# Kernel optimization log

Hardware: AMD Instinct MI355X
Metric: run time of the kernel (lower is better)

Reference implementation:

```python
import jax, jax.numpy as jnp
import numpy as np

B, S, D, H = 4, 2048, 1024, 16
DK = D // H
SCALE = 1.0 / np.float32(np.sqrt(DK))


def setup_inputs() -> dict:
    key = jax.random.key(0)
    ks = jax.random.split(key, 11)
    w = lambda k: (jax.random.normal(k, (D, D), jnp.float32) * 0.02)
    b = lambda k: (jax.random.normal(k, (D,), jnp.float32) * 0.02)
    return {
        "Q": jax.random.normal(ks[0], (B, S, D), jnp.float32),
        "K": jax.random.normal(ks[1], (B, S, D), jnp.float32),
        "V": jax.random.normal(ks[2], (B, S, D), jnp.float32),
        "Wq": w(ks[3]), "bq": b(ks[4]),
        "Wk": w(ks[5]), "bk": b(ks[6]),
        "Wv": w(ks[7]), "bv": b(ks[8]),
        "Wo": w(ks[9]), "bo": b(ks[10]),
        # causal mask, broadcast over batch and heads: [1,1,S,S]
        "mask": jnp.tril(jnp.ones((1, 1, S, S), dtype=bool)),
    }


def reference(Q, K, V, Wq, bq, Wk, bk, Wv, bv, Wo, bo, mask):
    def proj(x, W, bias):
        # [B,S,D] -> [B,H,S,DK]
        return (x @ W + bias).reshape(B, S, H, DK).transpose(0, 2, 1, 3)

    q = proj(Q, Wq, bq)
    k = proj(K, Wk, bk)
    v = proj(V, Wv, bv)
    scores = jnp.einsum("bhqd,bhkd->bhqk", q, k) * SCALE  # [B,H,S,S]
    scores = jnp.where(mask, scores, jnp.float32(-1e9))
    attn = jax.nn.softmax(scores, axis=-1)
    out = jnp.einsum("bhqk,bhkd->bhqd", attn, v)  # [B,H,S,DK]
    out = out.transpose(0, 2, 1, 3).reshape(B, S, D)
    return out @ Wo + bo
```

## Files before the change

kernel.cpp:

```cpp
#include <hip/hip_runtime.h>
#include <hip/hip_bf16.h>
#include <stdint.h>

#define BB 4
#define SS 2048
#define DD 1024
#define HH 16
#define DKK 64
#define MM (BB * SS)

typedef __hip_bfloat16 bf16;
typedef __attribute__((ext_vector_type(8))) short frag8;
typedef __attribute__((ext_vector_type(4))) float f32x4;

#define GLDS16(g, l)                                                        \
  __builtin_amdgcn_global_load_lds(                                         \
      (const __attribute__((address_space(1))) void*)(g),                   \
      (__attribute__((address_space(3))) void*)(l), 16, 0, 0)

#define MFMA __builtin_amdgcn_mfma_f32_16x16x32_bf16

__device__ __forceinline__ unsigned short f2bu(float f) {
  __hip_bfloat16 h = __float2bfloat16(f);
  return *reinterpret_cast<unsigned short*>(&h);
}

struct WtArgs {
  const float* s[3];
  unsigned short* d[3];
};
__global__ __launch_bounds__(256) void wtrans_kernel(WtArgs a) {
  const float* __restrict__ W = a.s[blockIdx.z];
  unsigned short* __restrict__ Wt = a.d[blockIdx.z];
  __shared__ float t[64][68];
  const int n0 = blockIdx.x * 64, k0 = blockIdx.y * 64;
  const int tid = threadIdx.x;
#pragma unroll
  for (int it = 0; it < 4; ++it) {
    const int kk = it * 16 + (tid >> 4);
    const int nn = (tid & 15) * 4;
    const float4 v = *(const float4*)&W[(size_t)(k0 + kk) * DD + n0 + nn];
    *(float4*)&t[kk][nn] = v;
  }
  __syncthreads();
#pragma unroll
  for (int it = 0; it < 2; ++it) {
    const int n = it * 32 + (tid >> 3);
    const int c = tid & 7;
    frag8 pk;
#pragma unroll
    for (int j = 0; j < 8; ++j) pk[j] = (short)f2bu(t[c * 8 + j][n]);
    *(frag8*)&Wt[(size_t)(n0 + n) * DD + k0 + c * 8] = pk;
  }
}

struct CvtArgs {
  const float* s[3];
  unsigned short* d[3];
};
__global__ __launch_bounds__(256) void cvt_kernel(CvtArgs a) {
  const float* __restrict__ src = a.s[blockIdx.y];
  unsigned short* __restrict__ dst = a.d[blockIdx.y];
  const size_t i = ((size_t)blockIdx.x * 256 + threadIdx.x) * 8;
  const float4 v0 = *(const float4*)&src[i];
  const float4 v1 = *(const float4*)&src[i + 4];
  frag8 pk;
  pk[0] = (short)f2bu(v0.x); pk[1] = (short)f2bu(v0.y);
  pk[2] = (short)f2bu(v0.z); pk[3] = (short)f2bu(v0.w);
  pk[4] = (short)f2bu(v1.x); pk[5] = (short)f2bu(v1.y);
  pk[6] = (short)f2bu(v1.z); pk[7] = (short)f2bu(v1.w);
  *(frag8*)&dst[i] = pk;
}

struct GArgs {
  const void* A[3];
  const unsigned short* W[3];
  const float* bias[3];
  void* out[3];
  float oscale[3];
  int abf16[3];
  int omode[3];
};
__global__ __launch_bounds__(256) void gemm_kernel(GArgs ga) {
  constexpr int K = DD;
  const int z = blockIdx.z;
  const void* __restrict__ Av = ga.A[z];
  const unsigned short* __restrict__ Wt = ga.W[z];
  const float* __restrict__ bias = ga.bias[z];
  void* __restrict__ outv = ga.out[z];
  const float oscale = ga.oscale[z];
  const int abf = ga.abf16[z];
  const int omode = ga.omode[z];

  __shared__ unsigned short Bs[2][128 * 64];
  __shared__ unsigned short As[2][128 * 64];
  const int tid = threadIdx.x;
  const int wave = tid >> 6, lane = tid & 63, quad = lane >> 4, l15 = lane & 15;
  const int wr = wave >> 1, wc = wave & 1;
  const int mt = blockIdx.x * 8 + (blockIdx.y >> 3);
  const int nt = blockIdx.y & 7;
  const int m0 = mt * 128, n0 = nt * 128;

  f32x4 acc[4][4] = {};
  float4 r0[4], r1[4];

  auto stageB = [&](int buf, int k0) {
#pragma unroll
    for (int c = 0; c < 4; ++c) {
      const int row = c * 32 + wave * 8 + (lane >> 3);
      const int gc = ((lane & 7) ^ (row & 7)) * 8;
      const unsigned short* g = &Wt[(size_t)(n0 + row) * K + k0 + gc];
      unsigned off = __builtin_amdgcn_readfirstlane(
          (unsigned)(buf * 16384 + (c * 32 + wave * 8) * 128));
      GLDS16(g, (char*)&Bs[0][0] + off);
    }
  };
  auto stageA16 = [&](int buf, int k0) {
    const unsigned short* A = (const unsigned short*)Av;
#pragma unroll
    for (int c = 0; c < 4; ++c) {
      const int row = c * 32 + wave * 8 + (lane >> 3);
      const int gc = ((lane & 7) ^ (row & 7)) * 8;
      const unsigned short* g = &A[(size_t)(m0 + row) * K + k0 + gc];
      unsigned off = __builtin_amdgcn_readfirstlane(
          (unsigned)(buf * 16384 + (c * 32 + wave * 8) * 128));
      GLDS16(g, (char*)&As[0][0] + off);
    }
  };
  auto loadA32 = [&](int k0) {
    const float* A = (const float*)Av;
#pragma unroll
    for (int it = 0; it < 4; ++it) {
      const int row = it * 32 + (tid >> 3);
      const int c = tid & 7;
      r0[it] = *(const float4*)&A[(size_t)(m0 + row) * K + k0 + c * 8];
      r1[it] = *(const float4*)&A[(size_t)(m0 + row) * K + k0 + c * 8 + 4];
    }
  };
  auto writeA32 = [&](int buf) {
#pragma unroll
    for (int it = 0; it < 4; ++it) {
      const int row = it * 32 + (tid >> 3);
      const int c = tid & 7;
      frag8 pk;
      pk[0] = (short)f2bu(r0[it].x); pk[1] = (short)f2bu(r0[it].y);
      pk[2] = (short)f2bu(r0[it].z); pk[3] = (short)f2bu(r0[it].w);
      pk[4] = (short)f2bu(r1[it].x); pk[5] = (short)f2bu(r1[it].y);
      pk[6] = (short)f2bu(r1[it].z); pk[7] = (short)f2bu(r1[it].w);
      *(frag8*)&As[buf][row * 64 + ((c ^ (row & 7)) * 8)] = pk;
    }
  };
  auto compute = [&](int buf) {
#pragma unroll
    for (int s = 0; s < 2; ++s) {
      frag8 af[4], bfr[4];
#pragma unroll
      for (int mi = 0; mi < 4; ++mi)
        af[mi] = *(const frag8*)&As[buf][(wr * 64 + mi * 16 + l15) * 64 +
                                         (((s * 4 + quad) ^ (l15 & 7)) * 8)];
#pragma unroll
      for (int ni = 0; ni < 4; ++ni)
        bfr[ni] = *(const frag8*)&Bs[buf][(wc * 64 + ni * 16 + l15) * 64 +
                                          (((s * 4 + quad) ^ (l15 & 7)) * 8)];
#pragma unroll
      for (int mi = 0; mi < 4; ++mi)
#pragma unroll
        for (int ni = 0; ni < 4; ++ni)
          acc[mi][ni] = MFMA(af[mi], bfr[ni], acc[mi][ni], 0, 0, 0);
    }
  };

  if (abf) {
    stageB(0, 0);
    stageA16(0, 0);
  } else {
    loadA32(0);
    stageB(0, 0);
    writeA32(0);
  }
  __syncthreads();

#pragma unroll 1
  for (int t = 0; t < 16; t += 2) {
    if (t + 1 < 16) {
      if (abf) {
        stageB(1, (t + 1) * 64);
        stageA16(1, (t + 1) * 64);
      } else {
        loadA32((t + 1) * 64);
        stageB(1, (t + 1) * 64);
      }
    }
    compute(0);
    if (!abf && t + 1 < 16) writeA32(1);
    __syncthreads();
    if (t + 2 < 16) {
      if (abf) {
        stageB(0, (t + 2) * 64);
        stageA16(0, (t + 2) * 64);
      } else {
        loadA32((t + 2) * 64);
        stageB(0, (t + 2) * 64);
      }
    }
    compute(1);
    if (!abf && t + 2 < 16) writeA32(0);
    __syncthreads();
  }

#pragma unroll
  for (int mi = 0; mi < 4; ++mi) {
#pragma unroll
    for (int ni = 0; ni < 4; ++ni) {
#pragma unroll
      for (int r = 0; r < 4; ++r) {
        const int grow = m0 + wr * 64 + mi * 16 + quad * 4 + r;
        const int gcol = n0 + wc * 64 + ni * 16 + l15;
        const float val = (acc[mi][ni][r] + bias[gcol]) * oscale;
        if (omode == 2) {
          ((float*)outv)[(size_t)grow * DD + gcol] = val;
        } else {
          const int b = grow / SS, s = grow % SS;
          const int h = gcol / DKK, dk = gcol % DKK;
          unsigned short* o = (unsigned short*)outv;
          if (omode == 0)
            o[(((size_t)(b * HH + h)) * SS + s) * DKK + dk] = f2bu(val);
          else
            o[(((size_t)(b * HH + h)) * DKK + dk) * SS + s] = f2bu(val);
        }
      }
    }
  }
}

__global__ __launch_bounds__(256) void fattn_kernel(
    const unsigned short* __restrict__ q, const unsigned short* __restrict__ k,
    const unsigned short* __restrict__ vt, unsigned short* __restrict__ ctx) {
  __shared__ unsigned short Ks[2][64 * 64];
  __shared__ unsigned short Vs[2][64 * 64];
  __shared__ unsigned short P_lds[4][16][36];
  const int tid = threadIdx.x;
  const int wave = tid >> 6, lane = tid & 63, quad = lane >> 4, l15 = lane & 15;
  const int bh = blockIdx.x & 63;
  const int tp = blockIdx.x >> 6;
  const size_t qkb = (size_t)bh * SS * DKK;
  const size_t vtb = (size_t)bh * DKK * SS;
  const int b = bh / HH, h = bh % HH;

  frag8 ones;
#pragma unroll
  for (int s = 0; s < 8; ++s) ones[s] = (short)0x3F80;

  auto stage = [&](int buf, int jt) {
#pragma unroll
    for (int c = 0; c < 2; ++c) {
      const int row = wave * 16 + c * 8 + (lane >> 3);
      const int gc = ((lane & 7) ^ (row & 7)) * 8;
      const unsigned short* g = &k[qkb + (size_t)(jt * 64 + row) * DKK + gc];
      unsigned off = __builtin_amdgcn_readfirstlane(
          (unsigned)(buf * 8192 + (wave * 16 + c * 8) * 128));
      GLDS16(g, (char*)&Ks[0][0] + off);
    }
#pragma unroll
    for (int c = 0; c < 2; ++c) {
      const int row = wave * 16 + c * 8 + (lane >> 3);
      const int gc = ((lane & 7) ^ (row & 7)) * 8;
      const unsigned short* g = &vt[vtb + (size_t)row * SS + jt * 64 + gc];
      unsigned off = __builtin_amdgcn_readfirstlane(
          (unsigned)(buf * 8192 + (wave * 16 + c * 8) * 128));
      GLDS16(g, (char*)&Vs[0][0] + off);
    }
  };

  for (int half = 0; half < 2; ++half) {
    const int t = half ? (31 - tp) : tp;
    const int q0 = t * 64 + wave * 16;

    const frag8 aq0 =
        *(const frag8*)&q[qkb + (size_t)(q0 + l15) * DKK + quad * 8];
    const frag8 aq1 =
        *(const frag8*)&q[qkb + (size_t)(q0 + l15) * DKK + 32 + quad * 8];

    f32x4 oacc[4] = {};
    f32x4 lacc = {};

    const int nT = t + 1;
    stage(0, 0);
    __syncthreads();

    for (int jt = 0; jt < nT; ++jt) {
      const int p = jt & 1;
      if (jt + 1 < nT) stage(1 - p, jt + 1);
      const bool diag = (jt == t);

#pragma unroll
      for (int jsub = 0; jsub < 2; ++jsub) {
        f32x4 sc[2];
#pragma unroll
        for (int g = 0; g < 2; ++g) {
          const int row = jsub * 32 + g * 16 + l15;
          const frag8 kf0 =
              *(const frag8*)&Ks[p][row * 64 + ((quad ^ (l15 & 7)) * 8)];
          const frag8 kf1 =
              *(const frag8*)&Ks[p][row * 64 + (((4 + quad) ^ (l15 & 7)) * 8)];
          f32x4 z = {};
          z = MFMA(aq0, kf0, z, 0, 0, 0);
          sc[g] = MFMA(aq1, kf1, z, 0, 0, 0);
        }
        float p0[4], p1[4];
        if (diag) {
          const int jg = jt * 64 + jsub * 32;
#pragma unroll
          for (int r = 0; r < 4; ++r) {
            const int ig = q0 + quad * 4 + r;
            p0[r] = (jg + l15 <= ig) ? __expf(sc[0][r]) : 0.f;
            p1[r] = (jg + 16 + l15 <= ig) ? __expf(sc[1][r]) : 0.f;
          }
        } else {
#pragma unroll
          for (int r = 0; r < 4; ++r) {
            p0[r] = __expf(sc[0][r]);
            p1[r] = __expf(sc[1][r]);
          }
        }
#pragma unroll
        for (int r = 0; r < 4; ++r) {
          P_lds[wave][quad * 4 + r][l15] = f2bu(p0[r]);
          P_lds[wave][quad * 4 + r][16 + l15] = f2bu(p1[r]);
        }
        const frag8 pa = *(const frag8*)&P_lds[wave][l15][quad * 8];
#pragma unroll
        for (int c = 0; c < 4; ++c) {
          const int vrow = c * 16 + l15;
          const int chunk = ((jsub * 4 + quad) ^ (l15 & 7));
          const frag8 vf = *(const frag8*)&Vs[p][vrow * 64 + chunk * 8];
          oacc[c] = MFMA(pa, vf, oacc[c], 0, 0, 0);
        }
        lacc = MFMA(pa, ones, lacc, 0, 0, 0);
      }
      __syncthreads();
    }

#pragma unroll
    for (int r = 0; r < 4; ++r) {
      const float inv = 1.f / lacc[r];
      const int ig = q0 + quad * 4 + r;
#pragma unroll
      for (int c = 0; c < 4; ++c)
        ctx[((size_t)(b * SS + ig)) * DD + h * DKK + c * 16 + l15] =
            f2bu(oacc[c][r] * inv);
    }
  }
}

extern "C" void kernel_launch(void* const* d_in, const int* in_sizes, int n_in,
                              void* d_out, int out_size, void* d_ws,
                              size_t ws_size, hipStream_t stream) {
  const float* Q = (const float*)d_in[0];
  const float* K = (const float*)d_in[1];
  const float* V = (const float*)d_in[2];
  const float* Wq = (const float*)d_in[3];
  const float* bq = (const float*)d_in[4];
  const float* Wk = (const float*)d_in[5];
  const float* bk = (const float*)d_in[6];
  const float* Wv = (const float*)d_in[7];
  const float* bv = (const float*)d_in[8];
  const float* Wo = (const float*)d_in[9];
  const float* bo = (const float*)d_in[10];

  const size_t NE = (size_t)MM * DD;
  unsigned short* ctx = (unsigned short*)d_ws;
  unsigned short* qp = ctx + NE;
  unsigned short* kp = qp + NE;
  unsigned short* vtp = kp + NE;
  unsigned short* Qb = vtp + NE;
  unsigned short* Kb = Qb + NE;
  unsigned short* Vb = Kb + NE;
  unsigned short* Wqt = ctx;
  unsigned short* Wkt = ctx + 1048576;
  unsigned short* Wvt = ctx + 2097152;
  unsigned short* Wot = qp;

  const bool fastQK = ws_size >= (size_t)6 * NE * sizeof(unsigned short);
  const bool fastV = ws_size >= (size_t)7 * NE * sizeof(unsigned short);

  const dim3 gg(8, 64, 3);

  WtArgs wa1;
  wa1.s[0] = Wq; wa1.s[1] = Wk; wa1.s[2] = Wv;
  wa1.d[0] = Wqt; wa1.d[1] = Wkt; wa1.d[2] = Wvt;
  wtrans_kernel<<<dim3(16, 16, 3), 256, 0, stream>>>(wa1);

  int ncvt = 0;
  CvtArgs ca;
  if (fastQK) {
    ca.s[0] = Q; ca.d[0] = Qb;
    ca.s[1] = K; ca.d[1] = Kb;
    ncvt = 2;
    if (fastV) { ca.s[2] = V; ca.d[2] = Vb; ncvt = 3; }
    cvt_kernel<<<dim3(NE / 2048, ncvt), 256, 0, stream>>>(ca);
  }

  GArgs g3;
  g3.A[0] = fastQK ? (const void*)Qb : (const void*)Q;
  g3.A[1] = fastQK ? (const void*)Kb : (const void*)K;
  g3.A[2] = fastV ? (const void*)Vb : (const void*)V;
  g3.W[0] = Wqt; g3.W[1] = Wkt; g3.W[2] = Wvt;
  g3.bias[0] = bq; g3.bias[1] = bk; g3.bias[2] = bv;
  g3.out[0] = qp; g3.out[1] = kp; g3.out[2] = vtp;
  g3.oscale[0] = 0.125f; g3.oscale[1] = 1.f; g3.oscale[2] = 1.f;
  g3.abf16[0] = fastQK ? 1 : 0; g3.abf16[1] = fastQK ? 1 : 0;
  g3.abf16[2] = fastV ? 1 : 0;
  g3.omode[0] = 0; g3.omode[1] = 0; g3.omode[2] = 1;
  gemm_kernel<<<gg, 256, 0, stream>>>(g3);

  fattn_kernel<<<dim3(BB * HH * 16), 256, 0, stream>>>(qp, kp, vtp, ctx);

  WtArgs wa2;
  wa2.s[0] = Wo; wa2.d[0] = Wot;
  wa2.s[1] = Wo; wa2.d[1] = Wot;
  wa2.s[2] = Wo; wa2.d[2] = Wot;
  wtrans_kernel<<<dim3(16, 16, 1), 256, 0, stream>>>(wa2);

  GArgs go;
  go.A[0] = (const void*)ctx; go.W[0] = Wot; go.bias[0] = bo;
  go.out[0] = (void*)d_out; go.oscale[0] = 1.f;
  go.abf16[0] = 1; go.omode[0] = 2;
  go.A[1] = go.A[0]; go.W[1] = go.W[0]; go.bias[1] = go.bias[0];
  go.out[1] = go.out[0]; go.oscale[1] = 1.f; go.abf16[1] = 1; go.omode[1] = 2;
  go.A[2] = go.A[0]; go.W[2] = go.W[0]; go.bias[2] = go.bias[0];
  go.out[2] = go.out[0]; go.oscale[2] = 1.f; go.abf16[2] = 1; go.omode[2] = 2;
  gemm_kernel<<<dim3(8, 64, 1), 256, 0, stream>>>(go);
}
```

Measured before the change: 361.9 us.

## Add BK=32 GEMM variant and widen attention blocks to 128 query rows

Adds a new bf16 GEMM kernel with K-tile of 32, a single-sync-per-step double buffer and a paired-row swizzled LDS layout, used for both projection and output GEMMs when the workspace is large enough. The attention kernel is changed to 512 threads (8 waves) covering 128 query rows per block, so each staged K/V tile is shared by twice as many waves. It also skips fully masked sub-tiles per wave and masks partially. Costs: more barriers in the GEMM and extra idle waves on diagonal tiles in attention.

```diff
diff --git a/kernel.cpp b/kernel.cpp
--- a/kernel.cpp
+++ b/kernel.cpp
@@ -81,6 +81,100 @@
   int abf16[3];
   int omode[3];
 };
+
+__global__ __launch_bounds__(256) void gemm32_kernel(GArgs ga) {
+  constexpr int K = DD;
+  const int z = blockIdx.z;
+  const unsigned short* __restrict__ A = (const unsigned short*)ga.A[z];
+  const unsigned short* __restrict__ Wt = ga.W[z];
+  const float* __restrict__ bias = ga.bias[z];
+  void* __restrict__ outv = ga.out[z];
+  const float oscale = ga.oscale[z];
+  const int omode = ga.omode[z];
+
+  __shared__ unsigned short As[2][128 * 32];
+  __shared__ unsigned short Bs[2][128 * 32];
+  const int tid = threadIdx.x;
+  const int wave = tid >> 6, lane = tid & 63, quad = lane >> 4, l15 = lane & 15;
+  const int wr = wave >> 1, wc = wave & 1;
+  const int mt = blockIdx.x * 8 + (blockIdx.y >> 3);
+  const int nt = blockIdx.y & 7;
+  const int m0 = mt * 128, n0 = nt * 128;
+
+  f32x4 acc[4][4] = {};
+
+  auto stage = [&](int buf, int k0) {
+#pragma unroll
+    for (int j = 0; j < 2; ++j) {
+      const int win = wave * 2 + j;
+      const int srl = lane >> 3;
+      const int pp = lane & 7;
+      const int p = pp ^ srl;
+      const int row = (win * 8 + srl) * 2 + (p >> 2);
+      const int c = p & 3;
+      const unsigned off = __builtin_amdgcn_readfirstlane(
+          (unsigned)(buf * 8192 + win * 1024));
+      GLDS16(&A[(size_t)(m0 + row) * K + k0 + c * 8], (char*)&As[0][0] + off);
+      GLDS16(&Wt[(size_t)(n0 + row) * K + k0 + c * 8], (char*)&Bs[0][0] + off);
+    }
+  };
+  auto compute = [&](int buf) {
+    frag8 af[4], bfr[4];
+#pragma unroll
+    for (int mi = 0; mi < 4; ++mi) {
+      const int R = wr * 64 + mi * 16 + l15;
+      const int sr = R >> 1;
+      const int pp = (((R & 1) << 2) | quad) ^ (sr & 7);
+      af[mi] = *(const frag8*)&As[buf][sr * 64 + pp * 8];
+    }
+#pragma unroll
+    for (int ni = 0; ni < 4; ++ni) {
+      const int R = wc * 64 + ni * 16 + l15;
+      const int sr = R >> 1;
+      const int pp = (((R & 1) << 2) | quad) ^ (sr & 7);
+      bfr[ni] = *(const frag8*)&Bs[buf][sr * 64 + pp * 8];
+    }
+#pragma unroll
+    for (int mi = 0; mi < 4; ++mi)
+#pragma unroll
+      for (int ni = 0; ni < 4; ++ni)
+        acc[mi][ni] = MFMA(af[mi], bfr[ni], acc[mi][ni], 0, 0, 0);
+  };
+
+  stage(0, 0);
+  __syncthreads();
+#pragma unroll 1
+  for (int t = 0; t < 32; ++t) {
+    if (t + 1 < 32) stage((t & 1) ^ 1, (t + 1) * 32);
+    compute(t & 1);
+    __syncthreads();
+  }
+
+#pragma unroll
+  for (int mi = 0; mi < 4; ++mi) {
+#pragma unroll
+    for (int ni = 0; ni < 4; ++ni) {
+#pragma unroll
+      for (int r = 0; r < 4; ++r) {
+        const int grow = m0 + wr * 64 + mi * 16 + quad * 4 + r;
+        const int gcol = n0 + wc * 64 + ni * 16 + l15;
+        const float val = (acc[mi][ni][r] + bias[gcol]) * oscale;
+        if (omode == 2) {
+          ((float*)outv)[(size_t)grow * DD + gcol] = val;
+        } else {
+          const int b = grow / SS, s = grow % SS;
+          const int h = gcol / DKK, dk = gcol % DKK;
+          unsigned short* outp = (unsigned short*)outv;
+          if (omode == 0)
+            outp[(((size_t)(b * HH + h)) * SS + s) * DKK + dk] = f2bu(val);
+          else
+            outp[(((size_t)(b * HH + h)) * DKK + dk) * SS + s] = f2bu(val);
+        }
+      }
+    }
+  }
+}
+
 __global__ __launch_bounds__(256) void gemm_kernel(GArgs ga) {
   constexpr int K = DD;
   const int z = blockIdx.z;
@@ -116,25 +210,25 @@
     }
   };
   auto stageA16 = [&](int buf, int k0) {
-    const unsigned short* A = (const unsigned short*)Av;
+    const unsigned short* Ap = (const unsigned short*)Av;
 #pragma unroll
     for (int c = 0; c < 4; ++c) {
       const int row = c * 32 + wave * 8 + (lane >> 3);
       const int gc = ((lane & 7) ^ (row & 7)) * 8;
-      const unsigned short* g = &A[(size_t)(m0 + row) * K + k0 + gc];
+      const unsigned short* g = &Ap[(size_t)(m0 + row) * K + k0 + gc];
       unsigned off = __builtin_amdgcn_readfirstlane(
           (unsigned)(buf * 16384 + (c * 32 + wave * 8) * 128));
       GLDS16(g, (char*)&As[0][0] + off);
     }
   };
   auto loadA32 = [&](int k0) {
-    const float* A = (const float*)Av;
+    const float* Ap = (const float*)Av;
 #pragma unroll
     for (int it = 0; it < 4; ++it) {
       const int row = it * 32 + (tid >> 3);
       const int c = tid & 7;
-      r0[it] = *(const float4*)&A[(size_t)(m0 + row) * K + k0 + c * 8];
-      r1[it] = *(const float4*)&A[(size_t)(m0 + row) * K + k0 + c * 8 + 4];
+      r0[it] = *(const float4*)&Ap[(size_t)(m0 + row) * K + k0 + c * 8];
+      r1[it] = *(const float4*)&Ap[(size_t)(m0 + row) * K + k0 + c * 8 + 4];
     }
   };
   auto writeA32 = [&](int buf) {
@@ -153,20 +247,20 @@
   auto compute = [&](int buf) {
 #pragma unroll
     for (int s = 0; s < 2; ++s) {
-      frag8 af[4], bfr[4];
+      frag8 a2[4], b2[4];
 #pragma unroll
       for (int mi = 0; mi < 4; ++mi)
-        af[mi] = *(const frag8*)&As[buf][(wr * 64 + mi * 16 + l15) * 64 +
+        a2[mi] = *(const frag8*)&As[buf][(wr * 64 + mi * 16 + l15) * 64 +
                                          (((s * 4 + quad) ^ (l15 & 7)) * 8)];
 #pragma unroll
       for (int ni = 0; ni < 4; ++ni)
-        bfr[ni] = *(const frag8*)&Bs[buf][(wc * 64 + ni * 16 + l15) * 64 +
-                                          (((s * 4 + quad) ^ (l15 & 7)) * 8)];
+        b2[ni] = *(const frag8*)&Bs[buf][(wc * 64 + ni * 16 + l15) * 64 +
+                                         (((s * 4 + quad) ^ (l15 & 7)) * 8)];
 #pragma unroll
       for (int mi = 0; mi < 4; ++mi)
 #pragma unroll
         for (int ni = 0; ni < 4; ++ni)
-          acc[mi][ni] = MFMA(af[mi], bfr[ni], acc[mi][ni], 0, 0, 0);
+          acc[mi][ni] = MFMA(a2[mi], b2[ni], acc[mi][ni], 0, 0, 0);
     }
   };
 
@@ -222,23 +316,23 @@
         } else {
           const int b = grow / SS, s = grow % SS;
           const int h = gcol / DKK, dk = gcol % DKK;
-          unsigned short* o = (unsigned short*)outv;
+          unsigned short* outp = (unsigned short*)outv;
           if (omode == 0)
-            o[(((size_t)(b * HH + h)) * SS + s) * DKK + dk] = f2bu(val);
+            outp[(((size_t)(b * HH + h)) * SS + s) * DKK + dk] = f2bu(val);
           else
-            o[(((size_t)(b * HH + h)) * DKK + dk) * SS + s] = f2bu(val);
+            outp[(((size_t)(b * HH + h)) * DKK + dk) * SS + s] = f2bu(val);
         }
       }
     }
   }
 }
 
-__global__ __launch_bounds__(256) void fattn_kernel(
+__global__ __launch_bounds__(512) void fattn_kernel(
     const unsigned short* __restrict__ q, const unsigned short* __restrict__ k,
     const unsigned short* __restrict__ vt, unsigned short* __restrict__ ctx) {
   __shared__ unsigned short Ks[2][64 * 64];
   __shared__ unsigned short Vs[2][64 * 64];
-  __shared__ unsigned short P_lds[4][16][36];
+  __shared__ unsigned short P_lds[8][16][36];
   const int tid = threadIdx.x;
   const int wave = tid >> 6, lane = tid & 63, quad = lane >> 4, l15 = lane & 15;
   const int bh = blockIdx.x & 63;
@@ -252,29 +346,18 @@
   for (int s = 0; s < 8; ++s) ones[s] = (short)0x3F80;
 
   auto stage = [&](int buf, int jt) {
-#pragma unroll
-    for (int c = 0; c < 2; ++c) {
-      const int row = wave * 16 + c * 8 + (lane >> 3);
-      const int gc = ((lane & 7) ^ (row & 7)) * 8;
-      const unsigned short* g = &k[qkb + (size_t)(jt * 64 + row) * DKK + gc];
-      unsigned off = __builtin_amdgcn_readfirstlane(
-          (unsigned)(buf * 8192 + (wave * 16 + c * 8) * 128));
-      GLDS16(g, (char*)&Ks[0][0] + off);
-    }
-#pragma unroll
-    for (int c = 0; c < 2; ++c) {
-      const int row = wave * 16 + c * 8 + (lane >> 3);
-      const int gc = ((lane & 7) ^ (row & 7)) * 8;
-      const unsigned short* g = &vt[vtb + (size_t)row * SS + jt * 64 + gc];
-      unsigned off = __builtin_amdgcn_readfirstlane(
-          (unsigned)(buf * 8192 + (wave * 16 + c * 8) * 128));
-      GLDS16(g, (char*)&Vs[0][0] + off);
-    }
+    const int row = wave * 8 + (lane >> 3);
+    const int gc = ((lane & 7) ^ (lane >> 3)) * 8;
+    const unsigned off =
+        __builtin_amdgcn_readfirstlane((unsigned)(buf * 8192 + wave * 1024));
+    GLDS16(&k[qkb + (size_t)(jt * 64 + row) * DKK + gc],
+           (char*)&Ks[0][0] + off);
+    GLDS16(&vt[vtb + (size_t)row * SS + jt * 64 + gc], (char*)&Vs[0][0] + off);
   };
 
   for (int half = 0; half < 2; ++half) {
-    const int t = half ? (31 - tp) : tp;
-    const int q0 = t * 64 + wave * 16;
+    const int t = half ? (15 - tp) : tp;
+    const int q0 = t * 128 + wave * 16;
 
     const frag8 aq0 =
         *(const frag8*)&q[qkb + (size_t)(q0 + l15) * DKK + quad * 8];
@@ -284,59 +367,62 @@
     f32x4 oacc[4] = {};
     f32x4 lacc = {};
 
-    const int nT = t + 1;
+    const int nT = 2 * t + 2;
     stage(0, 0);
     __syncthreads();
 
     for (int jt = 0; jt < nT; ++jt) {
       const int p = jt & 1;
       if (jt + 1 < nT) stage(1 - p, jt + 1);
-      const bool diag = (jt == t);
-
-#pragma unroll
-      for (int jsub = 0; jsub < 2; ++jsub) {
-        f32x4 sc[2];
-#pragma unroll
-        for (int g = 0; g < 2; ++g) {
-          const int row = jsub * 32 + g * 16 + l15;
-          const frag8 kf0 =
-              *(const frag8*)&Ks[p][row * 64 + ((quad ^ (l15 & 7)) * 8)];
-          const frag8 kf1 =
-              *(const frag8*)&Ks[p][row * 64 + (((4 + quad) ^ (l15 & 7)) * 8)];
-          f32x4 z = {};
-          z = MFMA(aq0, kf0, z, 0, 0, 0);
-          sc[g] = MFMA(aq1, kf1, z, 0, 0, 0);
+      const bool allmask = jt * 64 > q0 + 15;
+      const bool anymask = jt * 64 + 63 > q0;
+
+      if (!allmask) {
+#pragma unroll
+        for (int jsub = 0; jsub < 2; ++jsub) {
+          f32x4 sc[2];
+#pragma unroll
+          for (int g = 0; g < 2; ++g) {
+            const int row = jsub * 32 + g * 16 + l15;
+            const frag8 kf0 =
+                *(const frag8*)&Ks[p][row * 64 + ((quad ^ (l15 & 7)) * 8)];
+            const frag8 kf1 =
+                *(const frag8*)&Ks[p][row * 64 + (((4 + quad) ^ (l15 & 7)) * 8)];
+            f32x4 z = {};
+            z = MFMA(aq0, kf0, z, 0, 0, 0);
+            sc[g] = MFMA(aq1, kf1, z, 0, 0, 0);
+          }
+          float p0[4], p1[4];
+          if (anymask) {
+            const int jg = jt * 64 + jsub * 32;
+#pragma unroll
+            for (int r = 0; r < 4; ++r) {
+              const int ig = q0 + quad * 4 + r;
+              p0[r] = (jg + l15 <= ig) ? __expf(sc[0][r]) : 0.f;
+              p1[r] = (jg + 16 + l15 <= ig) ? __expf(sc[1][r]) : 0.f;
+            }
+          } else {
+#pragma unroll
+            for (int r = 0; r < 4; ++r) {
+              p0[r] = __expf(sc[0][r]);
+              p1[r] = __expf(sc[1][r]);
+            }
+          }
+#pragma unroll
+          for (int r = 0; r < 4; ++r) {
+            P_lds[wave][quad * 4 + r][l15] = f2bu(p0[r]);
+            P_lds[wave][quad * 4 + r][16 + l15] = f2bu(p1[r]);
+          }
+          const frag8 pa = *(const frag8*)&P_lds[wave][l15][quad * 8];
+#pragma unroll
+          for (int c = 0; c < 4; ++c) {
+            const int vrow = c * 16 + l15;
+            const int chunk = ((jsub * 4 + quad) ^ (l15 & 7));
+            const frag8 vf = *(const frag8*)&Vs[p][vrow * 64 + chunk * 8];
+            oacc[c] = MFMA(pa, vf, oacc[c], 0, 0, 0);
+          }
+          lacc = MFMA(pa, ones, lacc, 0, 0, 0);
         }
-        float p0[4], p1[4];
-        if (diag) {
-          const int jg = jt * 64 + jsub * 32;
-#pragma unroll
-          for (int r = 0; r < 4; ++r) {
-            const int ig = q0 + quad * 4 + r;
-            p0[r] = (jg + l15 <= ig) ? __expf(sc[0][r]) : 0.f;
-            p1[r] = (jg + 16 + l15 <= ig) ? __expf(sc[1][r]) : 0.f;
-          }
-        } else {
-#pragma unroll
-          for (int r = 0; r < 4; ++r) {
-            p0[r] = __expf(sc[0][r]);
-            p1[r] = __expf(sc[1][r]);
-          }
-        }
-#pragma unroll
-        for (int r = 0; r < 4; ++r) {
-          P_lds[wave][quad * 4 + r][l15] = f2bu(p0[r]);
-          P_lds[wave][quad * 4 + r][16 + l15] = f2bu(p1[r]);
-        }
-        const frag8 pa = *(const frag8*)&P_lds[wave][l15][quad * 8];
-#pragma unroll
-        for (int c = 0; c < 4; ++c) {
-          const int vrow = c * 16 + l15;
-          const int chunk = ((jsub * 4 + quad) ^ (l15 & 7));
-          const frag8 vf = *(const frag8*)&Vs[p][vrow * 64 + chunk * 8];
-          oacc[c] = MFMA(pa, vf, oacc[c], 0, 0, 0);
-        }
-        lacc = MFMA(pa, ones, lacc, 0, 0, 0);
       }
       __syncthreads();
     }
@@ -384,19 +470,16 @@
   const bool fastQK = ws_size >= (size_t)6 * NE * sizeof(unsigned short);
   const bool fastV = ws_size >= (size_t)7 * NE * sizeof(unsigned short);
 
-  const dim3 gg(8, 64, 3);
-
   WtArgs wa1;
   wa1.s[0] = Wq; wa1.s[1] = Wk; wa1.s[2] = Wv;
   wa1.d[0] = Wqt; wa1.d[1] = Wkt; wa1.d[2] = Wvt;
   wtrans_kernel<<<dim3(16, 16, 3), 256, 0, stream>>>(wa1);
 
-  int ncvt = 0;
   CvtArgs ca;
   if (fastQK) {
+    int ncvt = 2;
     ca.s[0] = Q; ca.d[0] = Qb;
     ca.s[1] = K; ca.d[1] = Kb;
-    ncvt = 2;
     if (fastV) { ca.s[2] = V; ca.d[2] = Vb; ncvt = 3; }
     cvt_kernel<<<dim3(NE / 2048, ncvt), 256, 0, stream>>>(ca);
   }
@@ -412,9 +495,13 @@
   g3.abf16[0] = fastQK ? 1 : 0; g3.abf16[1] = fastQK ? 1 : 0;
   g3.abf16[2] = fastV ? 1 : 0;
   g3.omode[0] = 0; g3.omode[1] = 0; g3.omode[2] = 1;
-  gemm_kernel<<<gg, 256, 0, stream>>>(g3);
-
-  fattn_kernel<<<dim3(BB * HH * 16), 256, 0, stream>>>(qp, kp, vtp, ctx);
+  if (fastV) {
+    gemm32_kernel<<<dim3(8, 64, 3), 256, 0, stream>>>(g3);
+  } else {
+    gemm_kernel<<<dim3(8, 64, 3), 256, 0, stream>>>(g3);
+  }
+
+  fattn_kernel<<<dim3(BB * HH * 8), 512, 0, stream>>>(qp, kp, vtp, ctx);
 
   WtArgs wa2;
   wa2.s[0] = Wo; wa2.d[0] = Wot;
@@ -430,5 +517,9 @@
   go.out[1] = go.out[0]; go.oscale[1] = 1.f; go.abf16[1] = 1; go.omode[1] = 2;
   go.A[2] = go.A[0]; go.W[2] = go.W[0]; go.bias[2] = go.bias[0];
   go.out[2] = go.out[0]; go.oscale[2] = 1.f; go.abf16[2] = 1; go.omode[2] = 2;
-  gemm_kernel<<<dim3(8, 64, 1), 256, 0, stream>>>(go);
-}
+  if (fastV) {
+    gemm32_kernel<<<dim3(8, 64, 1), 256, 0, stream>>>(go);
+  } else {
+    gemm_kernel<<<dim3(8, 64, 1), 256, 0, stream>>>(go);
+  }
+}
```

After: 356.0 us. About the same (-1.7%).
